# Performance work log

Hardware: AMD Instinct MI355X
Metric: run time of the kernel (lower is better)

## Reference

```python
import jax, jax.numpy as jnp
import numpy as np

B, S, D, F, E, TOP_K = 4, 2048, 1024, 4096, 8, 2

def setup_inputs() -> dict:
    key = jax.random.key(0)
    k0, k1, k2, k3 = jax.random.split(key, 4)
    x = jax.random.normal(k0, (B, S, D), dtype=jnp.float32)
    gate_w = jax.random.normal(k1, (E, D), dtype=jnp.float32) * 0.02  # nn.Linear(D,E,bias=False) weight [E,D]
    w1 = jax.random.normal(k2, (E, F, D), dtype=jnp.float32) * 0.02   # fc1 weight per expert [F,D]
    b1 = jnp.zeros((E, F), dtype=jnp.float32)
    w2 = jax.random.normal(k3, (E, D, F), dtype=jnp.float32) * 0.02   # fc2 weight per expert [D,F]
    b2 = jnp.zeros((E, D), dtype=jnp.float32)
    return {"x": x, "gate_w": gate_w, "w1": w1, "b1": b1, "w2": w2, "b2": b2}

def reference(x, gate_w, w1, b1, w2, b2):
    b, s, d = x.shape
    e = gate_w.shape[0]
    xf = x.reshape(-1, d)                      # [T, D]
    t = xf.shape[0]
    logits = xf @ gate_w.T                     # [T, E] (eval mode: no noise)
    probs = jax.nn.softmax(logits, axis=-1)
    top_v, top_i = jax.lax.top_k(probs, TOP_K)  # [T, K]
    top_v = top_v / (jnp.sum(top_v, axis=-1, keepdims=True) + 1e-9)
    # combine weights: scatter normalized top-k probs into a dense [T, E] table
    cw = jnp.zeros((t, e), dtype=xf.dtype).at[jnp.arange(t)[:, None], top_i].add(top_v)
    out = jnp.zeros_like(xf)
    for ei in range(e):  # fixed small expert loop; each expert FFN in eval mode (dropout inert)
        h = jax.nn.gelu(xf @ w1[ei].T + b1[ei], approximate=False)  # [T, F]
        y = h @ w2[ei].T + b2[ei]                                   # [T, D]
        out = out + cw[:, ei:ei + 1] * y
    return out.reshape(b, s, d), probs.reshape(b, s, e)
```

## Files before the change

kernel.cpp:

```cpp
#include <hip/hip_runtime.h>
#include <hip/hip_bf16.h>

typedef __attribute__((ext_vector_type(8))) short short8;
typedef __attribute__((ext_vector_type(4))) float f32x4;
typedef unsigned int uint;

#define T_TOK 8192
#define D_DIM 1024
#define F_DIM 4096
#define E_NUM 8
#define KTOP 2

__global__ void cvt_kernel(const float* __restrict__ in, short* __restrict__ out, int n8) {
    int i = blockIdx.x * blockDim.x + threadIdx.x;
    int stride = gridDim.x * blockDim.x;
    for (; i < n8; i += stride) {
        const float4* p = (const float4*)(in + (size_t)i * 8);
        float4 a = p[0], b = p[1];
        float va[8] = {a.x, a.y, a.z, a.w, b.x, b.y, b.z, b.w};
        short8 o;
#pragma unroll
        for (int j = 0; j < 8; ++j) {
            __hip_bfloat16 h = __float2bfloat16(va[j]);
            o[j] = *reinterpret_cast<short*>(&h);
        }
        *(short8*)(out + (size_t)i * 8) = o;
    }
}

__global__ void gate_kernel(const float* __restrict__ x, const float* __restrict__ gw,
                            float* __restrict__ probs, int4* __restrict__ idxrank,
                            float2* __restrict__ ww, int* __restrict__ counts) {
    const int lane = threadIdx.x & 63;
    const int wid = threadIdx.x >> 6;
    const int t = blockIdx.x * 4 + wid;
    const float4* xr = (const float4*)(x + (size_t)t * D_DIM);
    float acc[E_NUM];
#pragma unroll
    for (int e = 0; e < E_NUM; ++e) acc[e] = 0.f;
    for (int i = lane; i < D_DIM / 4; i += 64) {
        float4 xv = xr[i];
#pragma unroll
        for (int e = 0; e < E_NUM; ++e) {
            float4 gv = ((const float4*)(gw + (size_t)e * D_DIM))[i];
            acc[e] += xv.x * gv.x + xv.y * gv.y + xv.z * gv.z + xv.w * gv.w;
        }
    }
#pragma unroll
    for (int e = 0; e < E_NUM; ++e) {
#pragma unroll
        for (int off = 32; off > 0; off >>= 1) acc[e] += __shfl_xor(acc[e], off);
    }
    if (lane == 0) {
        float m = acc[0];
        for (int e = 1; e < E_NUM; ++e) m = fmaxf(m, acc[e]);
        float p[E_NUM], s = 0.f;
        for (int e = 0; e < E_NUM; ++e) { p[e] = expf(acc[e] - m); s += p[e]; }
        float inv = 1.f / s;
        for (int e = 0; e < E_NUM; ++e) {
            p[e] *= inv;
            probs[(size_t)t * E_NUM + e] = p[e];
        }
        float v0 = -1.f, v1 = -1.f; int i0 = 0, i1 = 0;
        for (int e = 0; e < E_NUM; ++e) {
            float v = p[e];
            if (v > v0) { v1 = v0; i1 = i0; v0 = v; i0 = e; }
            else if (v > v1) { v1 = v; i1 = e; }
        }
        float wsum = v0 + v1 + 1e-9f;
        int r0 = atomicAdd(&counts[i0], 1);
        int r1 = atomicAdd(&counts[i1], 1);
        idxrank[t] = make_int4(i0, i1, r0, r1);
        ww[t] = make_float2(v0 / wsum, v1 / wsum);
    }
}

__global__ void scan_kernel(const int* __restrict__ counts, int* __restrict__ offs) {
    if (threadIdx.x == 0 && blockIdx.x == 0) {
        int a = 0;
        for (int e = 0; e < E_NUM; ++e) { offs[e] = a; a += counts[e]; }
        offs[E_NUM] = a;
    }
}

__global__ void scatter_kernel(const int4* __restrict__ idxrank, const float2* __restrict__ ww,
                               const int* __restrict__ offs, int* __restrict__ token_list,
                               float* __restrict__ slot_w) {
    int t = blockIdx.x * blockDim.x + threadIdx.x;
    if (t >= T_TOK) return;
    int4 ir = idxrank[t];
    float2 w = ww[t];
    int s0 = offs[ir.x] + ir.z;
    int s1 = offs[ir.y] + ir.w;
    token_list[s0] = t; slot_w[s0] = w.x;
    token_list[s1] = t; slot_w[s1] = w.y;
}

__device__ __forceinline__ void gload16(const void* g, void* l) {
    __builtin_amdgcn_global_load_lds((const __attribute__((address_space(1))) uint*)g,
                                     (__attribute__((address_space(3))) uint*)l, 16, 0, 0);
}

__global__ void gemm1_kernel(const short* __restrict__ xb, const short* __restrict__ w1b,
                             const float* __restrict__ b1, const int* __restrict__ offs,
                             const int* __restrict__ token_list, short* __restrict__ H) {
    const int e = blockIdx.z, mt = blockIdx.y, nt = blockIdx.x;
    const int base = offs[e];
    const int cnt = offs[e + 1] - base;
    if (mt * 128 >= cnt) return;

    __shared__ __align__(16) short sA[128 * 32];
    __shared__ __align__(16) short sB[128 * 32];

    const int tid = threadIdx.x, wid = tid >> 6, lane = tid & 63;

    const short* srcA[2];
    const short* srcB[2];
#pragma unroll
    for (int j = 0; j < 2; ++j) {
        int c = j * 256 + tid;
        int row = c >> 2, c8 = c & 3;
        int slot = base + mt * 128 + row;
        int slotc = min(slot, base + cnt - 1);
        int tok = token_list[slotc];
        srcA[j] = xb + (size_t)tok * D_DIM + c8 * 8;
        srcB[j] = w1b + ((size_t)e * F_DIM + nt * 128 + row) * D_DIM + c8 * 8;
    }

    const int wm = wid >> 1, wn = wid & 1;
    const int fr = lane & 15, fk = lane >> 4;

    f32x4 acc[4][4];
#pragma unroll
    for (int i = 0; i < 4; ++i)
#pragma unroll
        for (int j = 0; j < 4; ++j) acc[i][j] = (f32x4){0.f, 0.f, 0.f, 0.f};

    for (int k0 = 0; k0 < D_DIM; k0 += 32) {
#pragma unroll
        for (int j = 0; j < 2; ++j) {
            gload16(srcA[j] + k0, &sA[(j * 256 + wid * 64) * 8]);
            gload16(srcB[j] + k0, &sB[(j * 256 + wid * 64) * 8]);
        }
        __syncthreads();
        short8 af[4], bfr[4];
#pragma unroll
        for (int i = 0; i < 4; ++i) af[i] = *(const short8*)&sA[(wm * 64 + i * 16 + fr) * 32 + fk * 8];
#pragma unroll
        for (int i = 0; i < 4; ++i) bfr[i] = *(const short8*)&sB[(wn * 64 + i * 16 + fr) * 32 + fk * 8];
#pragma unroll
        for (int i = 0; i < 4; ++i)
#pragma unroll
            for (int j = 0; j < 4; ++j)
                acc[i][j] = __builtin_amdgcn_mfma_f32_16x16x32_bf16(af[i], bfr[j], acc[i][j], 0, 0, 0);
        __syncthreads();
    }

#pragma unroll
    for (int i = 0; i < 4; ++i) {
        int mrow_base = mt * 128 + wm * 64 + i * 16 + (lane >> 4) * 4;
#pragma unroll
        for (int j = 0; j < 4; ++j) {
            int ncol = nt * 128 + wn * 64 + j * 16 + (lane & 15);
            float bias = b1[(size_t)e * F_DIM + ncol];
#pragma unroll
            for (int r = 0; r < 4; ++r) {
                int mrow = mrow_base + r;
                if (mrow < cnt) {
                    float v = acc[i][j][r] + bias;
                    v = 0.5f * v * (1.f + erff(v * 0.70710678118654752f));
                    __hip_bfloat16 h = __float2bfloat16(v);
                    H[(size_t)(base + mrow) * F_DIM + ncol] = *reinterpret_cast<short*>(&h);
                }
            }
        }
    }
}

__global__ void gemm2_kernel(const short* __restrict__ H, const short* __restrict__ w2b,
                             const float* __restrict__ b2, const int* __restrict__ offs,
                             const int* __restrict__ token_list, const float* __restrict__ slot_w,
                             float* __restrict__ out) {
    const int e = blockIdx.z, mt = blockIdx.y, nt = blockIdx.x;
    const int base = offs[e];
    const int cnt = offs[e + 1] - base;
    if (mt * 128 >= cnt) return;

    __shared__ __align__(16) short sA[128 * 32];
    __shared__ __align__(16) short sB[128 * 32];

    const int tid = threadIdx.x, wid = tid >> 6, lane = tid & 63;

    const short* srcA[2];
    const short* srcB[2];
#pragma unroll
    for (int j = 0; j < 2; ++j) {
        int c = j * 256 + tid;
        int row = c >> 2, c8 = c & 3;
        int slotc = min(base + mt * 128 + row, base + cnt - 1);
        srcA[j] = H + (size_t)slotc * F_DIM + c8 * 8;
        srcB[j] = w2b + ((size_t)e * D_DIM + nt * 128 + row) * F_DIM + c8 * 8;
    }

    const int wm = wid >> 1, wn = wid & 1;
    const int fr = lane & 15, fk = lane >> 4;

    f32x4 acc[4][4];
#pragma unroll
    for (int i = 0; i < 4; ++i)
#pragma unroll
        for (int j = 0; j < 4; ++j) acc[i][j] = (f32x4){0.f, 0.f, 0.f, 0.f};

    for (int k0 = 0; k0 < F_DIM; k0 += 32) {
#pragma unroll
        for (int j = 0; j < 2; ++j) {
            gload16(srcA[j] + k0, &sA[(j * 256 + wid * 64) * 8]);
            gload16(srcB[j] + k0, &sB[(j * 256 + wid * 64) * 8]);
        }
        __syncthreads();
        short8 af[4], bfr[4];
#pragma unroll
        for (int i = 0; i < 4; ++i) af[i] = *(const short8*)&sA[(wm * 64 + i * 16 + fr) * 32 + fk * 8];
#pragma unroll
        for (int i = 0; i < 4; ++i) bfr[i] = *(const short8*)&sB[(wn * 64 + i * 16 + fr) * 32 + fk * 8];
#pragma unroll
        for (int i = 0; i < 4; ++i)
#pragma unroll
            for (int j = 0; j < 4; ++j)
                acc[i][j] = __builtin_amdgcn_mfma_f32_16x16x32_bf16(af[i], bfr[j], acc[i][j], 0, 0, 0);
        __syncthreads();
    }

#pragma unroll
    for (int i = 0; i < 4; ++i) {
        int mrow_base = mt * 128 + wm * 64 + i * 16 + (lane >> 4) * 4;
#pragma unroll
        for (int r = 0; r < 4; ++r) {
            int mrow = mrow_base + r;
            if (mrow < cnt) {
                int slot = base + mrow;
                int tok = token_list[slot];
                float w = slot_w[slot];
#pragma unroll
                for (int j = 0; j < 4; ++j) {
                    int ncol = nt * 128 + wn * 64 + j * 16 + (lane & 15);
                    float v = (acc[i][j][r] + b2[(size_t)e * D_DIM + ncol]) * w;
                    atomicAdd(&out[(size_t)tok * D_DIM + ncol], v);
                }
            }
        }
    }
}

extern "C" void kernel_launch(void* const* d_in, const int* in_sizes, int n_in,
                              void* d_out, int out_size, void* d_ws, size_t ws_size,
                              hipStream_t stream) {
    const float* x      = (const float*)d_in[0];
    const float* gate_w = (const float*)d_in[1];
    const float* w1     = (const float*)d_in[2];
    const float* b1     = (const float*)d_in[3];
    const float* w2     = (const float*)d_in[4];
    const float* b2     = (const float*)d_in[5];

    float* out   = (float*)d_out;
    float* probs = out + (size_t)T_TOK * D_DIM;

    char* w = (char*)d_ws;
    int* counts = (int*)w;
    int* offs   = (int*)(w + 64);
    size_t off = 256;
    int4*   idxrank    = (int4*)(w + off);  off += (size_t)T_TOK * 16;
    float2* ww_        = (float2*)(w + off); off += (size_t)T_TOK * 8;
    int*    token_list = (int*)(w + off);   off += (size_t)T_TOK * KTOP * 4;
    float*  slot_w     = (float*)(w + off); off += (size_t)T_TOK * KTOP * 4;
    short*  xb  = (short*)(w + off); off += (size_t)T_TOK * D_DIM * 2;
    short*  w1b = (short*)(w + off); off += (size_t)E_NUM * F_DIM * D_DIM * 2;
    short*  w2b = (short*)(w + off); off += (size_t)E_NUM * D_DIM * F_DIM * 2;
    short*  H   = (short*)(w + off); off += (size_t)T_TOK * KTOP * F_DIM * 2;
    (void)ws_size;

    hipMemsetAsync(out, 0, (size_t)T_TOK * D_DIM * sizeof(float), stream);
    hipMemsetAsync(counts, 0, 64, stream);

    cvt_kernel<<<2048, 256, 0, stream>>>(x, xb, T_TOK * D_DIM / 8);
    cvt_kernel<<<4096, 256, 0, stream>>>(w1, w1b, E_NUM * F_DIM * D_DIM / 8);
    cvt_kernel<<<4096, 256, 0, stream>>>(w2, w2b, E_NUM * D_DIM * F_DIM / 8);

    gate_kernel<<<T_TOK / 4, 256, 0, stream>>>(x, gate_w, probs, idxrank, ww_, counts);
    scan_kernel<<<1, 64, 0, stream>>>(counts, offs);
    scatter_kernel<<<T_TOK / 256, 256, 0, stream>>>(idxrank, ww_, offs, token_list, slot_w);

    gemm1_kernel<<<dim3(F_DIM / 128, T_TOK / 128, E_NUM), 256, 0, stream>>>(
        xb, w1b, b1, offs, token_list, H);
    gemm2_kernel<<<dim3(D_DIM / 128, T_TOK / 128, E_NUM), 256, 0, stream>>>(
        H, w2b, b2, offs, token_list, slot_w, out);
}
```

Measured before the change: 1.082 ms.

## Rewrite expert GEMMs with 256x256 tiles, LDS pipeline, split-K and XCD swizzle

Both expert GEMMs now use 512-thread blocks with 256x256 output tiles and a 4-deep LDS ring filled by async global-to-LDS loads two k-steps ahead. They use explicit barriers, wait counts and MFMA priority hints to overlap loads with matrix math. Blocks are remapped so neighbouring tiles land on the same XCD, and gemm2 splits K in two, relying on the existing atomics. The x-to-bf16 conversion is folded into the gate kernel, removing one launch and a reread of x. The larger tiles raise register pressure and LDS use, and the split-K doubles atomic traffic on the output.

After: 1.176 ms. 1.09x slower.

```diff
diff --git a/kernel.cpp b/kernel.cpp
--- a/kernel.cpp
+++ b/kernel.cpp
@@ -10,6 +10,15 @@
 #define F_DIM 4096
 #define E_NUM 8
 #define KTOP 2
+
+__device__ __forceinline__ int xcd_swizzle(int bid, int nwg) {
+    return (bid & 7) * (nwg >> 3) + (bid >> 3);
+}
+
+__device__ __forceinline__ short bf16bits(float v) {
+    __hip_bfloat16 h = __float2bfloat16(v);
+    return *reinterpret_cast<short*>(&h);
+}
 
 __global__ void cvt_kernel(const float* __restrict__ in, short* __restrict__ out, int n8) {
     int i = blockIdx.x * blockDim.x + threadIdx.x;
@@ -20,17 +29,15 @@
         float va[8] = {a.x, a.y, a.z, a.w, b.x, b.y, b.z, b.w};
         short8 o;
 #pragma unroll
-        for (int j = 0; j < 8; ++j) {
-            __hip_bfloat16 h = __float2bfloat16(va[j]);
-            o[j] = *reinterpret_cast<short*>(&h);
-        }
+        for (int j = 0; j < 8; ++j) o[j] = bf16bits(va[j]);
         *(short8*)(out + (size_t)i * 8) = o;
     }
 }
 
 __global__ void gate_kernel(const float* __restrict__ x, const float* __restrict__ gw,
                             float* __restrict__ probs, int4* __restrict__ idxrank,
-                            float2* __restrict__ ww, int* __restrict__ counts) {
+                            float2* __restrict__ ww, int* __restrict__ counts,
+                            short* __restrict__ xb) {
     const int lane = threadIdx.x & 63;
     const int wid = threadIdx.x >> 6;
     const int t = blockIdx.x * 4 + wid;
@@ -40,6 +47,10 @@
     for (int e = 0; e < E_NUM; ++e) acc[e] = 0.f;
     for (int i = lane; i < D_DIM / 4; i += 64) {
         float4 xv = xr[i];
+        short4 s;
+        s.x = bf16bits(xv.x); s.y = bf16bits(xv.y);
+        s.z = bf16bits(xv.z); s.w = bf16bits(xv.w);
+        *(short4*)(xb + (size_t)t * D_DIM + i * 4) = s;
 #pragma unroll
         for (int e = 0; e < E_NUM; ++e) {
             float4 gv = ((const float4*)(gw + (size_t)e * D_DIM))[i];
@@ -101,151 +112,203 @@
                                      (__attribute__((address_space(3))) uint*)l, 16, 0, 0);
 }
 
-__global__ void gemm1_kernel(const short* __restrict__ xb, const short* __restrict__ w1b,
-                             const float* __restrict__ b1, const int* __restrict__ offs,
-                             const int* __restrict__ token_list, short* __restrict__ H) {
-    const int e = blockIdx.z, mt = blockIdx.y, nt = blockIdx.x;
+#define SBAR() __builtin_amdgcn_s_barrier()
+#define SCHEDB() __builtin_amdgcn_sched_barrier(0)
+#define WAITV4() asm volatile("s_waitcnt vmcnt(4)" ::: "memory")
+#define WAITV0() asm volatile("s_waitcnt vmcnt(0)" ::: "memory")
+
+
+#define STAGE(op, ptr, t)                                                     \
+    do {                                                                      \
+        short* d_ = &lds[(t) & 3][op][half * 256 + row_s][0];                 \
+        const short* s_ = (ptr) + (t) * 32;                                   \
+        gload16(s_, d_);                                                      \
+        gload16(s_ + 16, d_ + 512 * 8);                                       \
+    } while (0)
+
+#define LOAD_A(mq)                                                            \
+    {                                                                         \
+        const short* At = &lds[t & 3][0][0][0];                               \
+        _Pragma("unroll")                                                     \
+        for (int m = 0; m < 4; ++m)                                           \
+            av[m] = *(const short8*)&At[(fk4 * 256 + wm * 128 + (mq) * 64 +   \
+                                         m * 16 + fr) * 8];                   \
+    }
+
+#define LOAD_B()                                                              \
+    {                                                                         \
+        const short* Bt = &lds[t & 3][1][0][0];                               \
+        _Pragma("unroll")                                                     \
+        for (int n = 0; n < 4; ++n)                                           \
+            bv[n] = *(const short8*)&Bt[(fk4 * 256 + wn * 64 + n * 16 + fr) * 8]; \
+    }
+
+#define MFMA16(mq)                                                            \
+    __builtin_amdgcn_s_setprio(1);                                            \
+    _Pragma("unroll")                                                         \
+    for (int m = 0; m < 4; ++m)                                               \
+        _Pragma("unroll")                                                     \
+        for (int n = 0; n < 4; ++n)                                           \
+            acc[(mq) * 4 + m][n] = __builtin_amdgcn_mfma_f32_16x16x32_bf16(   \
+                av[m], bv[n], acc[(mq) * 4 + m][n], 0, 0, 0);                 \
+    __builtin_amdgcn_s_setprio(0);
+
+__global__ void __launch_bounds__(512, 2)
+gemm1_kernel(const short* __restrict__ xb, const short* __restrict__ w1b,
+             const float* __restrict__ b1, const int* __restrict__ offs,
+             const int* __restrict__ token_list, short* __restrict__ H) {
+    const int nwg = 32 * 16 * E_NUM;
+    int sid = xcd_swizzle(blockIdx.x, nwg);
+    const int mt = sid & 31;
+    const int nt = (sid >> 5) & 15;
+    const int e  = sid >> 9;
+
     const int base = offs[e];
     const int cnt = offs[e + 1] - base;
-    if (mt * 128 >= cnt) return;
-
-    __shared__ __align__(16) short sA[128 * 32];
-    __shared__ __align__(16) short sB[128 * 32];
-
-    const int tid = threadIdx.x, wid = tid >> 6, lane = tid & 63;
-
-    const short* srcA[2];
-    const short* srcB[2];
-#pragma unroll
-    for (int j = 0; j < 2; ++j) {
-        int c = j * 256 + tid;
-        int row = c >> 2, c8 = c & 3;
-        int slot = base + mt * 128 + row;
-        int slotc = min(slot, base + cnt - 1);
-        int tok = token_list[slotc];
-        srcA[j] = xb + (size_t)tok * D_DIM + c8 * 8;
-        srcB[j] = w1b + ((size_t)e * F_DIM + nt * 128 + row) * D_DIM + c8 * 8;
-    }
-
-    const int wm = wid >> 1, wn = wid & 1;
-    const int fr = lane & 15, fk = lane >> 4;
-
-    f32x4 acc[4][4];
-#pragma unroll
-    for (int i = 0; i < 4; ++i)
-#pragma unroll
-        for (int j = 0; j < 4; ++j) acc[i][j] = (f32x4){0.f, 0.f, 0.f, 0.f};
-
-    for (int k0 = 0; k0 < D_DIM; k0 += 32) {
-#pragma unroll
-        for (int j = 0; j < 2; ++j) {
-            gload16(srcA[j] + k0, &sA[(j * 256 + wid * 64) * 8]);
-            gload16(srcB[j] + k0, &sB[(j * 256 + wid * 64) * 8]);
-        }
-        __syncthreads();
-        short8 af[4], bfr[4];
-#pragma unroll
-        for (int i = 0; i < 4; ++i) af[i] = *(const short8*)&sA[(wm * 64 + i * 16 + fr) * 32 + fk * 8];
-#pragma unroll
-        for (int i = 0; i < 4; ++i) bfr[i] = *(const short8*)&sB[(wn * 64 + i * 16 + fr) * 32 + fk * 8];
-#pragma unroll
-        for (int i = 0; i < 4; ++i)
-#pragma unroll
-            for (int j = 0; j < 4; ++j)
-                acc[i][j] = __builtin_amdgcn_mfma_f32_16x16x32_bf16(af[i], bfr[j], acc[i][j], 0, 0, 0);
-        __syncthreads();
-    }
-
-#pragma unroll
-    for (int i = 0; i < 4; ++i) {
-        int mrow_base = mt * 128 + wm * 64 + i * 16 + (lane >> 4) * 4;
-#pragma unroll
-        for (int j = 0; j < 4; ++j) {
-            int ncol = nt * 128 + wn * 64 + j * 16 + (lane & 15);
-            float bias = b1[(size_t)e * F_DIM + ncol];
-#pragma unroll
-            for (int r = 0; r < 4; ++r) {
-                int mrow = mrow_base + r;
-                if (mrow < cnt) {
-                    float v = acc[i][j][r] + bias;
+    if (mt * 256 >= cnt) return;
+
+    __shared__ __align__(16) short lds[4][2][1024][8];
+
+    const int tid = threadIdx.x;
+    const int wid = tid >> 6, lane = tid & 63;
+    const int wm = wid >> 2, wn = wid & 3;
+    const int fr = lane & 15, fk4 = lane >> 4;
+    const int row_s = tid & 255, half = tid >> 8;
+
+    int slotc = min(base + mt * 256 + row_s, base + cnt - 1);
+    int tok = token_list[slotc];
+    const short* aptr = xb + (size_t)tok * D_DIM + half * 8;
+    const short* bptr = w1b + ((size_t)e * F_DIM + nt * 256 + row_s) * D_DIM + half * 8;
+
+    f32x4 acc[8][4];
+#pragma unroll
+    for (int m = 0; m < 8; ++m)
+#pragma unroll
+        for (int n = 0; n < 4; ++n) acc[m][n] = (f32x4){0.f, 0.f, 0.f, 0.f};
+
+    const int NT = D_DIM / 32;
+    STAGE(0, aptr, 0); STAGE(1, bptr, 0);
+    STAGE(0, aptr, 1); STAGE(1, bptr, 1);
+    WAITV4();
+    SBAR();
+    SCHEDB();
+
+    for (int t = 0; t < NT; ++t) {
+        short8 av[4], bv[4];
+        LOAD_A(0); LOAD_B();
+        if (t + 2 < NT) STAGE(0, aptr, t + 2);
+        SBAR();
+        MFMA16(0);
+        SBAR();
+        LOAD_A(1);
+        if (t + 2 < NT) STAGE(1, bptr, t + 2);
+        SBAR();
+        MFMA16(1);
+        if (t < NT - 1) {
+            if (t + 2 < NT) WAITV4(); else WAITV0();
+        }
+        SBAR();
+        SCHEDB();
+    }
+
+    float bias[4];
+#pragma unroll
+    for (int n = 0; n < 4; ++n)
+        bias[n] = b1[(size_t)e * F_DIM + nt * 256 + wn * 64 + n * 16 + fr];
+#pragma unroll
+    for (int m = 0; m < 8; ++m) {
+        int grow = mt * 256 + wm * 128 + m * 16 + fk4 * 4;
+#pragma unroll
+        for (int r = 0; r < 4; ++r) {
+            if (grow + r < cnt) {
+                size_t rowoff = (size_t)(base + grow + r) * F_DIM + nt * 256 + wn * 64 + fr;
+#pragma unroll
+                for (int n = 0; n < 4; ++n) {
+                    float v = acc[m][n][r] + bias[n];
                     v = 0.5f * v * (1.f + erff(v * 0.70710678118654752f));
-                    __hip_bfloat16 h = __float2bfloat16(v);
-                    H[(size_t)(base + mrow) * F_DIM + ncol] = *reinterpret_cast<short*>(&h);
+                    H[rowoff + n * 16] = bf16bits(v);
                 }
             }
         }
     }
 }
 
-__global__ void gemm2_kernel(const short* __restrict__ H, const short* __restrict__ w2b,
-                             const float* __restrict__ b2, const int* __restrict__ offs,
-                             const int* __restrict__ token_list, const float* __restrict__ slot_w,
-                             float* __restrict__ out) {
-    const int e = blockIdx.z, mt = blockIdx.y, nt = blockIdx.x;
+__global__ void __launch_bounds__(512, 2)
+gemm2_kernel(const short* __restrict__ H, const short* __restrict__ w2b,
+             const float* __restrict__ b2, const int* __restrict__ offs,
+             const int* __restrict__ token_list, const float* __restrict__ slot_w,
+             float* __restrict__ out) {
+    const int nwg = 4 * 32 * 2 * E_NUM;
+    int sid = xcd_swizzle(blockIdx.x, nwg);
+    const int nt = sid & 3;
+    const int mt = (sid >> 2) & 31;
+    const int ks = (sid >> 7) & 1;
+    const int e  = sid >> 8;
+
     const int base = offs[e];
     const int cnt = offs[e + 1] - base;
-    if (mt * 128 >= cnt) return;
-
-    __shared__ __align__(16) short sA[128 * 32];
-    __shared__ __align__(16) short sB[128 * 32];
-
-    const int tid = threadIdx.x, wid = tid >> 6, lane = tid & 63;
-
-    const short* srcA[2];
-    const short* srcB[2];
-#pragma unroll
-    for (int j = 0; j < 2; ++j) {
-        int c = j * 256 + tid;
-        int row = c >> 2, c8 = c & 3;
-        int slotc = min(base + mt * 128 + row, base + cnt - 1);
-        srcA[j] = H + (size_t)slotc * F_DIM + c8 * 8;
-        srcB[j] = w2b + ((size_t)e * D_DIM + nt * 128 + row) * F_DIM + c8 * 8;
-    }
-
-    const int wm = wid >> 1, wn = wid & 1;
-    const int fr = lane & 15, fk = lane >> 4;
-
-    f32x4 acc[4][4];
-#pragma unroll
-    for (int i = 0; i < 4; ++i)
-#pragma unroll
-        for (int j = 0; j < 4; ++j) acc[i][j] = (f32x4){0.f, 0.f, 0.f, 0.f};
-
-    for (int k0 = 0; k0 < F_DIM; k0 += 32) {
-#pragma unroll
-        for (int j = 0; j < 2; ++j) {
-            gload16(srcA[j] + k0, &sA[(j * 256 + wid * 64) * 8]);
-            gload16(srcB[j] + k0, &sB[(j * 256 + wid * 64) * 8]);
-        }
-        __syncthreads();
-        short8 af[4], bfr[4];
-#pragma unroll
-        for (int i = 0; i < 4; ++i) af[i] = *(const short8*)&sA[(wm * 64 + i * 16 + fr) * 32 + fk * 8];
-#pragma unroll
-        for (int i = 0; i < 4; ++i) bfr[i] = *(const short8*)&sB[(wn * 64 + i * 16 + fr) * 32 + fk * 8];
-#pragma unroll
-        for (int i = 0; i < 4; ++i)
-#pragma unroll
-            for (int j = 0; j < 4; ++j)
-                acc[i][j] = __builtin_amdgcn_mfma_f32_16x16x32_bf16(af[i], bfr[j], acc[i][j], 0, 0, 0);
-        __syncthreads();
-    }
-
-#pragma unroll
-    for (int i = 0; i < 4; ++i) {
-        int mrow_base = mt * 128 + wm * 64 + i * 16 + (lane >> 4) * 4;
+    if (mt * 256 >= cnt) return;
+
+    __shared__ __align__(16) short lds[4][2][1024][8];
+
+    const int tid = threadIdx.x;
+    const int wid = tid >> 6, lane = tid & 63;
+    const int wm = wid >> 2, wn = wid & 3;
+    const int fr = lane & 15, fk4 = lane >> 4;
+    const int row_s = tid & 255, half = tid >> 8;
+
+    int slotc = min(base + mt * 256 + row_s, base + cnt - 1);
+    const short* aptr = H + (size_t)slotc * F_DIM + ks * 2048 + half * 8;
+    const short* bptr = w2b + ((size_t)e * D_DIM + nt * 256 + row_s) * F_DIM + ks * 2048 + half * 8;
+
+    f32x4 acc[8][4];
+#pragma unroll
+    for (int m = 0; m < 8; ++m)
+#pragma unroll
+        for (int n = 0; n < 4; ++n) acc[m][n] = (f32x4){0.f, 0.f, 0.f, 0.f};
+
+    const int NT = 2048 / 32;
+    STAGE(0, aptr, 0); STAGE(1, bptr, 0);
+    STAGE(0, aptr, 1); STAGE(1, bptr, 1);
+    WAITV4();
+    SBAR();
+    SCHEDB();
+
+    for (int t = 0; t < NT; ++t) {
+        short8 av[4], bv[4];
+        LOAD_A(0); LOAD_B();
+        if (t + 2 < NT) STAGE(0, aptr, t + 2);
+        SBAR();
+        MFMA16(0);
+        SBAR();
+        LOAD_A(1);
+        if (t + 2 < NT) STAGE(1, bptr, t + 2);
+        SBAR();
+        MFMA16(1);
+        if (t < NT - 1) {
+            if (t + 2 < NT) WAITV4(); else WAITV0();
+        }
+        SBAR();
+        SCHEDB();
+    }
+
+    float b2v[4];
+#pragma unroll
+    for (int n = 0; n < 4; ++n)
+        b2v[n] = (ks == 0) ? b2[(size_t)e * D_DIM + nt * 256 + wn * 64 + n * 16 + fr] : 0.f;
+#pragma unroll
+    for (int m = 0; m < 8; ++m) {
+        int grow = mt * 256 + wm * 128 + m * 16 + fk4 * 4;
 #pragma unroll
         for (int r = 0; r < 4; ++r) {
-            int mrow = mrow_base + r;
-            if (mrow < cnt) {
-                int slot = base + mrow;
+            if (grow + r < cnt) {
+                int slot = base + grow + r;
                 int tok = token_list[slot];
                 float w = slot_w[slot];
-#pragma unroll
-                for (int j = 0; j < 4; ++j) {
-                    int ncol = nt * 128 + wn * 64 + j * 16 + (lane & 15);
-                    float v = (acc[i][j][r] + b2[(size_t)e * D_DIM + ncol]) * w;
-                    atomicAdd(&out[(size_t)tok * D_DIM + ncol], v);
+                float* orow = out + (size_t)tok * D_DIM + nt * 256 + wn * 64 + fr;
+#pragma unroll
+                for (int n = 0; n < 4; ++n) {
+                    atomicAdd(&orow[n * 16], (acc[m][n][r] + b2v[n]) * w);
                 }
             }
         }
@@ -282,16 +345,15 @@
     hipMemsetAsync(out, 0, (size_t)T_TOK * D_DIM * sizeof(float), stream);
     hipMemsetAsync(counts, 0, 64, stream);
 
-    cvt_kernel<<<2048, 256, 0, stream>>>(x, xb, T_TOK * D_DIM / 8);
     cvt_kernel<<<4096, 256, 0, stream>>>(w1, w1b, E_NUM * F_DIM * D_DIM / 8);
     cvt_kernel<<<4096, 256, 0, stream>>>(w2, w2b, E_NUM * D_DIM * F_DIM / 8);
 
-    gate_kernel<<<T_TOK / 4, 256, 0, stream>>>(x, gate_w, probs, idxrank, ww_, counts);
+    gate_kernel<<<T_TOK / 4, 256, 0, stream>>>(x, gate_w, probs, idxrank, ww_, counts, xb);
     scan_kernel<<<1, 64, 0, stream>>>(counts, offs);
     scatter_kernel<<<T_TOK / 256, 256, 0, stream>>>(idxrank, ww_, offs, token_list, slot_w);
 
-    gemm1_kernel<<<dim3(F_DIM / 128, T_TOK / 128, E_NUM), 256, 0, stream>>>(
+    gemm1_kernel<<<32 * 16 * E_NUM, 512, 0, stream>>>(
         xb, w1b, b1, offs, token_list, H);
-    gemm2_kernel<<<dim3(D_DIM / 128, T_TOK / 128, E_NUM), 256, 0, stream>>>(
+    gemm2_kernel<<<4 * 32 * 2 * E_NUM, 512, 0, stream>>>(
         H, w2b, b2, offs, token_list, slot_w, out);
 }
```
